# Performance work log

Measured on AMD Instinct MI355X. Metric: run time of the kernel, lower is better.

Reference implementation:

```python
import jax, jax.numpy as jnp
import numpy as np

EPS_LN = 1e-5
ALPHA_THRESH = 1.0 / 255.0


def _make_coord(X, Y):
    # make_coord((X,Y), flatten=True): centers in [-1,1], row-major over (X,Y)
    cx = (jnp.arange(X, dtype=jnp.float32) + 0.5) / X * 2.0 - 1.0
    cy = (jnp.arange(Y, dtype=jnp.float32) + 0.5) / Y * 2.0 - 1.0
    gx, gy = jnp.meshgrid(cx, cy, indexing='ij')
    return jnp.stack([gx.reshape(-1), gy.reshape(-1)], axis=-1)  # [X*Y, 2]


def _mlp(x, w1, b1, w2, b2):
    return jax.nn.relu(x @ w1 + b1) @ w2 + b2


def _unfold3x3(feat):
    # feat: [B,C,X,Y] -> torch F.unfold(3, padding=1) layout [B, C*9, X, Y]
    B, C, X, Y = feat.shape
    fp = jnp.pad(feat, ((0, 0), (0, 0), (1, 1), (1, 1)))
    patches = jnp.stack([fp[:, :, ki:ki + X, kj:kj + Y]
                         for ki in range(3) for kj in range(3)], axis=2)  # [B,C,9,X,Y]
    return patches.reshape(B, C * 9, X, Y)


def _render_one(xy, scale, rot, color, H, W):
    # project_gaussians_2d_scale_rot: ndc -> pixel centers
    cx = 0.5 * ((xy[:, 0] + 1.0) * W - 1.0)  # [N]
    cy = 0.5 * ((xy[:, 1] + 1.0) * H - 1.0)
    c, s = jnp.cos(rot[:, 0]), jnp.sin(rot[:, 0])
    sx2, sy2 = scale[:, 0] ** 2, scale[:, 1] ** 2
    cov00 = c * c * sx2 + s * s * sy2
    cov01 = c * s * (sx2 - sy2)
    cov11 = s * s * sx2 + c * c * sy2
    det = cov00 * cov11 - cov01 * cov01
    A = cov11 / det   # conic xx
    Bc = -cov01 / det  # conic xy
    Cc = cov00 / det  # conic yy
    px = jnp.arange(W, dtype=jnp.float32)
    py = jnp.arange(H, dtype=jnp.float32)
    dx = px[None, :, None] - cx[None, None, :]  # [1,W,N] -> broadcast [H,W,N]
    dy = py[:, None, None] - cy[None, None, :]  # [H,1,N]
    sigma = 0.5 * (A * dx * dx + Cc * dy * dy) + Bc * dx * dy  # [H,W,N]
    alpha = jnp.exp(-sigma)  # opacity = 1
    alpha = jnp.where(alpha >= ALPHA_THRESH, alpha, 0.0)  # rasterizer skip threshold
    img = jnp.einsum('hwn,nc->hwc', alpha, color)  # sum-compositing
    img = jnp.clip(img, 0.0, 1.0)
    return jnp.transpose(img, (2, 0, 1))  # [3,H,W]


def reference(inp, conv_w, conv_b,
              off_w1, off_b1, off_w2, off_b2,
              sc_w1, sc_b1, sc_w2, sc_b2,
              rot_w1, rot_b1, rot_w2, rot_b2,
              col_w1, col_b1, col_w2, col_b2,
              target_h, target_w):
    H0, W0 = inp.shape[-2], inp.shape[-1]
    factor = max(target_h / H0, target_w / W0)
    # encoder: 3x3 conv, same padding
    feat = jax.lax.conv_general_dilated(
        inp, conv_w, (1, 1), 'SAME',
        dimension_numbers=('NCHW', 'OIHW', 'NCHW')) + conv_b[None, :, None, None]
    feat = jnp.transpose(feat, (0, 1, 3, 2))  # [B,C,X=W0,Y=H0]
    B, C, X, Y = feat.shape
    feat = _unfold3x3(feat)  # [B,C*9,X,Y]
    feat = jnp.transpose(feat, (0, 2, 3, 1)).reshape(B, X * Y, C * 9)
    mu = jnp.mean(feat, axis=-1, keepdims=True)
    var = jnp.var(feat, axis=-1, keepdims=True)
    feat = (feat - mu) / jnp.sqrt(var + EPS_LN)
    coord = _make_coord(X, Y)[None]  # [1,N,2]
    off_factor = 2.0 * factor / max(target_h, target_w)
    offset = jnp.tanh(_mlp(feat, off_w1, off_b1, off_w2, off_b2)) * 3.0 * off_factor
    xy = coord + offset                                               # [B,N,2]
    scale = jax.nn.sigmoid(_mlp(feat, sc_w1, sc_b1, sc_w2, sc_b2)) * 2.0 * factor
    rot = jax.nn.sigmoid(_mlp(feat, rot_w1, rot_b1, rot_w2, rot_b2)) * 2.0 * jnp.pi
    color = jnp.tanh(_mlp(feat, col_w1, col_b1, col_w2, col_b2))
    render = jax.vmap(lambda a, b, c2, d: _render_one(a, b, c2, d, target_h, target_w))
    return render(xy, scale, rot, color)  # [B,3,H,W]


def setup_inputs() -> dict:
    key = jax.random.key(0)
    ks = jax.random.split(key, 16)
    d_in, hid = 288, 256

    def lin(k, fan_in, shape):
        return jax.random.normal(k, shape, jnp.float32) / np.sqrt(fan_in)

    return {
        'inp': jax.random.uniform(ks[0], (1, 3, 48, 48), jnp.float32),
        'conv_w': lin(ks[1], 27, (32, 3, 3, 3)),
        'conv_b': jnp.zeros((32,), jnp.float32),
        'off_w1': lin(ks[2], d_in, (d_in, hid)), 'off_b1': jnp.zeros((hid,), jnp.float32),
        'off_w2': lin(ks[3], hid, (hid, 2)), 'off_b2': jnp.zeros((2,), jnp.float32),
        'sc_w1': lin(ks[4], d_in, (d_in, hid)), 'sc_b1': jnp.zeros((hid,), jnp.float32),
        'sc_w2': lin(ks[5], hid, (hid, 2)), 'sc_b2': jnp.zeros((2,), jnp.float32),
        'rot_w1': lin(ks[6], d_in, (d_in, hid)), 'rot_b1': jnp.zeros((hid,), jnp.float32),
        'rot_w2': lin(ks[7], hid, (hid, 1)), 'rot_b2': jnp.zeros((1,), jnp.float32),
        'col_w1': lin(ks[8], d_in, (d_in, hid)), 'col_b1': jnp.zeros((hid,), jnp.float32),
        'col_w2': lin(ks[9], hid, (hid, 3)), 'col_b2': jnp.zeros((3,), jnp.float32),
        'target_h': 192,
        'target_w': 192,
    }
```

## Files before the change

### kernel.cpp

```cpp
#include <hip/hip_runtime.h>

#define NXY   48
#define NG    2304
#define CFE   32
#define KDIM  288
#define HID   256
#define NHID  1024
#define HW    192
#define NPIX  (HW*HW)
#define NCHUNK (NG/64)

typedef __bf16 bf16x8 __attribute__((ext_vector_type(8)));
typedef float  f32x4  __attribute__((ext_vector_type(4)));
typedef unsigned short ushort_t;
typedef unsigned int   uint_t;

__device__ __forceinline__ ushort_t f2bf(float x) {
    uint_t u = __float_as_uint(x);
    uint_t r = u + 0x7FFFu + ((u >> 16) & 1u);
    return (ushort_t)(r >> 16);
}
__device__ __forceinline__ float bf2f(ushort_t h) {
    return __uint_as_float(((uint_t)h) << 16);
}

__global__ __launch_bounds__(256) void conv_k(const float* __restrict__ inp,
                                              const float* __restrict__ cw,
                                              const float* __restrict__ cb,
                                              float* __restrict__ feat) {
    int idx = blockIdx.x * 256 + threadIdx.x;
    if (idx >= CFE * NXY * NXY) return;
    int w = idx % NXY, h = (idx / NXY) % NXY, o = idx / (NXY * NXY);
    float acc = cb[o];
    #pragma unroll
    for (int i = 0; i < 3; ++i) {
        #pragma unroll
        for (int kh = 0; kh < 3; ++kh) {
            int hh = h + kh - 1;
            if (hh < 0 || hh >= NXY) continue;
            #pragma unroll
            for (int kw = 0; kw < 3; ++kw) {
                int ww = w + kw - 1;
                if (ww < 0 || ww >= NXY) continue;
                acc = fmaf(inp[(i * NXY + hh) * NXY + ww],
                           cw[((o * 3 + i) * 3 + kh) * 3 + kw], acc);
            }
        }
    }
    feat[idx] = acc;
}

__global__ __launch_bounds__(64) void ln_k(const float* __restrict__ feat,
                                           ushort_t* __restrict__ Ahi,
                                           ushort_t* __restrict__ Alo) {
    int n = blockIdx.x;
    int lane = threadIdx.x;
    int x = n / NXY, y = n % NXY;
    float v[5];
    float sum = 0.f, sq = 0.f;
    #pragma unroll
    for (int i = 0; i < 5; ++i) {
        int k = lane + 64 * i;
        float val = 0.f;
        if (k < KDIM) {
            int c = k / 9, r = k % 9, ki = r / 3, kj = r % 3;
            int hh = y + kj - 1, ww = x + ki - 1;
            if (hh >= 0 && hh < NXY && ww >= 0 && ww < NXY)
                val = feat[(c * NXY + hh) * NXY + ww];
        }
        v[i] = val; sum += val; sq = fmaf(val, val, sq);
    }
    #pragma unroll
    for (int off = 32; off; off >>= 1) {
        sum += __shfl_xor(sum, off);
        sq  += __shfl_xor(sq,  off);
    }
    float mean = sum * (1.0f / KDIM);
    float var  = sq * (1.0f / KDIM) - mean * mean;
    float rstd = rsqrtf(var + 1e-5f);
    #pragma unroll
    for (int i = 0; i < 5; ++i) {
        int k = lane + 64 * i;
        if (k < KDIM) {
            float w = (v[i] - mean) * rstd;
            ushort_t hb = f2bf(w);
            ushort_t lb = f2bf(w - bf2f(hb));
            Ahi[n * KDIM + k] = hb;
            Alo[n * KDIM + k] = lb;
        }
    }
}

__global__ __launch_bounds__(256) void w1pack_k(const float* __restrict__ w0,
        const float* __restrict__ w1, const float* __restrict__ w2,
        const float* __restrict__ w3,
        ushort_t* __restrict__ Bph, ushort_t* __restrict__ Bpl) {
    int tid = blockIdx.x * 256 + threadIdx.x;
    if (tid >= 64 * 9 * 64) return;
    int l = tid & 63;
    int t = tid >> 6;
    int ks = t % 9, nf = t / 9;
    int ncol = nf * 16 + (l & 15);
    int head = ncol >> 8, c = ncol & 255;
    const float* w = head == 0 ? w0 : head == 1 ? w1 : head == 2 ? w2 : w3;
    int kbase = ks * 32 + (l >> 4) * 8;
    ushort_t hb[8], lb[8];
    #pragma unroll
    for (int i = 0; i < 8; ++i) {
        float x = w[(kbase + i) * HID + c];
        hb[i] = f2bf(x);
        lb[i] = f2bf(x - bf2f(hb[i]));
    }
    #pragma unroll
    for (int i = 0; i < 8; ++i) {
        Bph[tid * 8 + i] = hb[i];
        Bpl[tid * 8 + i] = lb[i];
    }
}

__global__ __launch_bounds__(256) void gemm_k(const ushort_t* __restrict__ Ahi,
        const ushort_t* __restrict__ Alo,
        const ushort_t* __restrict__ Bph, const ushort_t* __restrict__ Bpl,
        const float* __restrict__ b1_0, const float* __restrict__ b1_1,
        const float* __restrict__ b1_2, const float* __restrict__ b1_3,
        float* __restrict__ Hout) {
    int l   = threadIdx.x & 63;
    int wv  = threadIdx.x >> 6;
    int m0  = blockIdx.x * 64 + (wv >> 1) * 32;
    int nf0 = blockIdx.y * 4 + (wv & 1) * 2;
    int r15 = l & 15, kg = l >> 4;
    f32x4 acc[2][2] = {};
    const ushort_t* pah = Ahi + (m0 + r15) * KDIM + kg * 8;
    const ushort_t* pal = Alo + (m0 + r15) * KDIM + kg * 8;
    #pragma unroll 3
    for (int ks = 0; ks < 9; ++ks) {
        bf16x8 ah[2], al[2], bh[2], bl[2];
        #pragma unroll
        for (int m = 0; m < 2; ++m) {
            ah[m] = *(const bf16x8*)(pah + m * 16 * KDIM + ks * 32);
            al[m] = *(const bf16x8*)(pal + m * 16 * KDIM + ks * 32);
        }
        #pragma unroll
        for (int n = 0; n < 2; ++n) {
            size_t off = ((size_t)((nf0 + n) * 9 + ks) * 64 + l) * 8;
            bh[n] = *(const bf16x8*)(Bph + off);
            bl[n] = *(const bf16x8*)(Bpl + off);
        }
        #pragma unroll
        for (int m = 0; m < 2; ++m)
            #pragma unroll
            for (int n = 0; n < 2; ++n) {
                acc[m][n] = __builtin_amdgcn_mfma_f32_16x16x32_bf16(ah[m], bh[n], acc[m][n], 0, 0, 0);
                acc[m][n] = __builtin_amdgcn_mfma_f32_16x16x32_bf16(ah[m], bl[n], acc[m][n], 0, 0, 0);
                acc[m][n] = __builtin_amdgcn_mfma_f32_16x16x32_bf16(al[m], bh[n], acc[m][n], 0, 0, 0);
            }
    }
    #pragma unroll
    for (int n = 0; n < 2; ++n) {
        int col = (nf0 + n) * 16 + r15;
        int head = col >> 8;
        const float* bb = head == 0 ? b1_0 : head == 1 ? b1_1 : head == 2 ? b1_2 : b1_3;
        float bias = bb[col & 255];
        #pragma unroll
        for (int m = 0; m < 2; ++m)
            #pragma unroll
            for (int r = 0; r < 4; ++r) {
                int grow = m0 + m * 16 + kg * 4 + r;
                Hout[grow * NHID + col] = fmaxf(acc[m][n][r] + bias, 0.f);
            }
    }
}

__global__ __launch_bounds__(256) void head_k(const float* __restrict__ Hh,
        const float* __restrict__ ow2, const float* __restrict__ ob2,
        const float* __restrict__ sw2, const float* __restrict__ sb2,
        const float* __restrict__ rw2, const float* __restrict__ rb2,
        const float* __restrict__ cw2, const float* __restrict__ cb2,
        float4* __restrict__ gbox, float4* __restrict__ gdat) {
    int tid = threadIdx.x;
    int lane = tid & 63, wv = tid >> 6;
    int n = blockIdx.x * 4 + wv;
    const float* h = Hh + n * NHID;
    float s[8] = {};
    #pragma unroll
    for (int i = 0; i < 4; ++i) {
        int j = lane + 64 * i;
        float h0 = h[j], h1 = h[256 + j], h2 = h[512 + j], h3 = h[768 + j];
        s[0] = fmaf(h0, ow2[j * 2 + 0], s[0]);
        s[1] = fmaf(h0, ow2[j * 2 + 1], s[1]);
        s[2] = fmaf(h1, sw2[j * 2 + 0], s[2]);
        s[3] = fmaf(h1, sw2[j * 2 + 1], s[3]);
        s[4] = fmaf(h2, rw2[j],         s[4]);
        s[5] = fmaf(h3, cw2[j * 3 + 0], s[5]);
        s[6] = fmaf(h3, cw2[j * 3 + 1], s[6]);
        s[7] = fmaf(h3, cw2[j * 3 + 2], s[7]);
    }
    #pragma unroll
    for (int off = 32; off; off >>= 1)
        #pragma unroll
        for (int k = 0; k < 8; ++k) s[k] += __shfl_xor(s[k], off);
    if (lane == 0) {
        float o0 = s[0] + ob2[0], o1 = s[1] + ob2[1];
        float z0 = s[2] + sb2[0], z1 = s[3] + sb2[1];
        float zr = s[4] + rb2[0];
        float c0 = s[5] + cb2[0], c1 = s[6] + cb2[1], c2 = s[7] + cb2[2];
        int x = n / NXY, y = n % NXY;
        float ndcx = ((x + 0.5f) * (2.0f / NXY) - 1.0f) + tanhf(o0) * 0.125f;
        float ndcy = ((y + 0.5f) * (2.0f / NXY) - 1.0f) + tanhf(o1) * 0.125f;
        float cxp = 0.5f * ((ndcx + 1.0f) * HW - 1.0f);
        float cyp = 0.5f * ((ndcy + 1.0f) * HW - 1.0f);
        float sx = 8.0f / (1.0f + expf(-z0));
        float sy = 8.0f / (1.0f + expf(-z1));
        float rot = 6.283185307179586f / (1.0f + expf(-zr));
        float cc = cosf(rot), ss = sinf(rot);
        float sx2 = sx * sx, sy2 = sy * sy;
        float cov00 = cc * cc * sx2 + ss * ss * sy2;
        float cov01 = cc * ss * (sx2 - sy2);
        float cov11 = ss * ss * sx2 + cc * cc * sy2;
        float det = cov00 * cov11 - cov01 * cov01;
        float inv = 1.0f / det;
        float A = cov11 * inv, Bc = -cov01 * inv, Cc = cov00 * inv;
        float rx = sqrtf(11.2f * cov00) + 1e-2f;
        float ry = sqrtf(11.2f * cov11) + 1e-2f;
        gbox[n]         = make_float4(cxp, cyp, rx, ry);
        gdat[2 * n]     = make_float4(0.5f * A, Bc, 0.5f * Cc, tanhf(c0));
        gdat[2 * n + 1] = make_float4(tanhf(c1), tanhf(c2), 0.f, 0.f);
    }
}

__global__ __launch_bounds__(256) void render_k(const float4* __restrict__ gbox,
                                                const float4* __restrict__ gdat,
                                                float* __restrict__ out) {
    __shared__ float4 ldsE[4][64][2];
    __shared__ float red[4][64][3];
    int lane = threadIdx.x & 63;
    int wv   = threadIdx.x >> 6;
    int tx0 = blockIdx.x * 8, ty0 = blockIdx.y * 8;
    float px = (float)(tx0 + (lane & 7));
    float py = (float)(ty0 + (lane >> 3));
    float xlo = (float)tx0, xhi = (float)(tx0 + 7);
    float ylo = (float)ty0, yhi = (float)(ty0 + 7);
    float ar = 0.f, ag = 0.f, ab = 0.f;
    for (int c = wv; c < NCHUNK; c += 4) {
        int g = c * 64 + lane;
        float4 bb = gbox[g];
        bool pred = (bb.x - bb.z <= xhi) && (bb.x + bb.z >= xlo) &&
                    (bb.y - bb.w <= yhi) && (bb.y + bb.w >= ylo);
        unsigned long long m = __ballot(pred);
        int cnt = __popcll(m);
        int pos = __popcll(m & ((1ull << lane) - 1ull));
        if (pred) {
            float4 d0 = gdat[2 * g];
            float4 d1 = gdat[2 * g + 1];
            ldsE[wv][pos][0] = make_float4(bb.x, bb.y, d0.x, d0.y);
            ldsE[wv][pos][1] = make_float4(d0.z, d0.w, d1.x, d1.y);
        }
        __syncthreads();
        for (int i = 0; i < cnt; ++i) {
            float4 e0 = ldsE[wv][i][0];
            float4 e1 = ldsE[wv][i][1];
            float dx = px - e0.x;
            float dy = py - e0.y;
            float sigma = fmaf(dx, fmaf(e0.z, dx, e0.w * dy), e1.x * dy * dy);
            float a = __expf(-sigma);
            a = (a >= (1.0f / 255.0f)) ? a : 0.f;
            ar = fmaf(a, e1.y, ar);
            ag = fmaf(a, e1.z, ag);
            ab = fmaf(a, e1.w, ab);
        }
        __syncthreads();
    }
    red[wv][lane][0] = ar; red[wv][lane][1] = ag; red[wv][lane][2] = ab;
    __syncthreads();
    if (wv == 0) {
        float r_ = red[0][lane][0] + red[1][lane][0] + red[2][lane][0] + red[3][lane][0];
        float g_ = red[0][lane][1] + red[1][lane][1] + red[2][lane][1] + red[3][lane][1];
        float b_ = red[0][lane][2] + red[1][lane][2] + red[2][lane][2] + red[3][lane][2];
        int pix = (ty0 + (lane >> 3)) * HW + tx0 + (lane & 7);
        out[pix]            = fminf(fmaxf(r_, 0.f), 1.f);
        out[NPIX + pix]     = fminf(fmaxf(g_, 0.f), 1.f);
        out[2 * NPIX + pix] = fminf(fmaxf(b_, 0.f), 1.f);
    }
}

extern "C" void kernel_launch(void* const* d_in, const int* in_sizes, int n_in,
                              void* d_out, int out_size, void* d_ws, size_t ws_size,
                              hipStream_t stream) {
    const float* inp = (const float*)d_in[0];
    const float* cw  = (const float*)d_in[1];
    const float* cb  = (const float*)d_in[2];
    const float* ow1 = (const float*)d_in[3];
    const float* ob1 = (const float*)d_in[4];
    const float* ow2 = (const float*)d_in[5];
    const float* ob2 = (const float*)d_in[6];
    const float* sw1 = (const float*)d_in[7];
    const float* sb1 = (const float*)d_in[8];
    const float* sw2 = (const float*)d_in[9];
    const float* sb2 = (const float*)d_in[10];
    const float* rw1 = (const float*)d_in[11];
    const float* rb1 = (const float*)d_in[12];
    const float* rw2 = (const float*)d_in[13];
    const float* rb2 = (const float*)d_in[14];
    const float* cw1 = (const float*)d_in[15];
    const float* cb1 = (const float*)d_in[16];
    const float* cw2 = (const float*)d_in[17];
    const float* cb2 = (const float*)d_in[18];

    float* ws = (float*)d_ws;
    float*    feat = ws;
    float*    hid  = ws + 73728;
    float4*   gbox = (float4*)(ws + 2433024);
    float4*   gdat = (float4*)(ws + 2442240);
    ushort_t* Ahi  = (ushort_t*)(ws + 2460672);
    ushort_t* Alo  = (ushort_t*)(ws + 2792448);
    ushort_t* Bph  = (ushort_t*)(ws + 3124224);
    ushort_t* Bpl  = (ushort_t*)(ws + 3271680);
    float* out = (float*)d_out;

    hipLaunchKernelGGL(conv_k, dim3(288), dim3(256), 0, stream, inp, cw, cb, feat);
    hipLaunchKernelGGL(ln_k, dim3(NG), dim3(64), 0, stream, feat, Ahi, Alo);
    hipLaunchKernelGGL(w1pack_k, dim3(144), dim3(256), 0, stream,
                       ow1, sw1, rw1, cw1, Bph, Bpl);
    hipLaunchKernelGGL(gemm_k, dim3(36, 16), dim3(256), 0, stream,
                       Ahi, Alo, Bph, Bpl, ob1, sb1, rb1, cb1, hid);
    hipLaunchKernelGGL(head_k, dim3(576), dim3(256), 0, stream,
                       hid, ow2, ob2, sw2, sb2, rw2, rb2, cw2, cb2, gbox, gdat);
    hipLaunchKernelGGL(render_k, dim3(24, 24), dim3(256), 0, stream, gbox, gdat, out);
}
```

Baseline: 47.30 us.

## Split-K the hidden GEMM into two partials and drop render barriers

The first-layer GEMM grid gains a z dimension that splits the 9 K-steps into two ranges. Each half writes its raw partial sums to a separate buffer, and head_k now adds the two partials plus the bias and applies ReLU. This doubles the number of GEMM blocks to fill more CUs, at the cost of twice the hidden-activation write and read traffic. Separately, render_k replaces its block-wide __syncthreads around the per-wave LDS staging with an LDS waitcnt, because each wave only reads its own ldsE slice.

```diff
diff --git a/kernel.cpp b/kernel.cpp
--- a/kernel.cpp
+++ b/kernel.cpp
@@ -118,22 +118,13 @@
     }
 }
 
-__global__ __launch_bounds__(256) void gemm_k(const ushort_t* __restrict__ Ahi,
-        const ushort_t* __restrict__ Alo,
+template<int KB, int KE>
+__device__ __forceinline__ void gemm_core(const ushort_t* __restrict__ pah,
+        const ushort_t* __restrict__ pal,
         const ushort_t* __restrict__ Bph, const ushort_t* __restrict__ Bpl,
-        const float* __restrict__ b1_0, const float* __restrict__ b1_1,
-        const float* __restrict__ b1_2, const float* __restrict__ b1_3,
-        float* __restrict__ Hout) {
-    int l   = threadIdx.x & 63;
-    int wv  = threadIdx.x >> 6;
-    int m0  = blockIdx.x * 64 + (wv >> 1) * 32;
-    int nf0 = blockIdx.y * 4 + (wv & 1) * 2;
-    int r15 = l & 15, kg = l >> 4;
-    f32x4 acc[2][2] = {};
-    const ushort_t* pah = Ahi + (m0 + r15) * KDIM + kg * 8;
-    const ushort_t* pal = Alo + (m0 + r15) * KDIM + kg * 8;
-    #pragma unroll 3
-    for (int ks = 0; ks < 9; ++ks) {
+        int nf0, int l, f32x4 acc[2][2]) {
+    #pragma unroll
+    for (int ks = KB; ks < KE; ++ks) {
         bf16x8 ah[2], al[2], bh[2], bl[2];
         #pragma unroll
         for (int m = 0; m < 2; ++m) {
@@ -155,23 +146,40 @@
                 acc[m][n] = __builtin_amdgcn_mfma_f32_16x16x32_bf16(al[m], bh[n], acc[m][n], 0, 0, 0);
             }
     }
+}
+
+__global__ __launch_bounds__(256, 4) void gemm_k(const ushort_t* __restrict__ Ahi,
+        const ushort_t* __restrict__ Alo,
+        const ushort_t* __restrict__ Bph, const ushort_t* __restrict__ Bpl,
+        float* __restrict__ HP) {
+    int l   = threadIdx.x & 63;
+    int wv  = threadIdx.x >> 6;
+    int kz  = blockIdx.z;
+    int m0  = blockIdx.x * 64 + (wv >> 1) * 32;
+    int nf0 = blockIdx.y * 4 + (wv & 1) * 2;
+    int r15 = l & 15, kg = l >> 4;
+    f32x4 acc[2][2] = {};
+    const ushort_t* pah = Ahi + (m0 + r15) * KDIM + kg * 8;
+    const ushort_t* pal = Alo + (m0 + r15) * KDIM + kg * 8;
+    if (kz == 0) gemm_core<0, 4>(pah, pal, Bph, Bpl, nf0, l, acc);
+    else         gemm_core<4, 9>(pah, pal, Bph, Bpl, nf0, l, acc);
+    float* out = HP + (size_t)kz * NG * NHID;
     #pragma unroll
     for (int n = 0; n < 2; ++n) {
         int col = (nf0 + n) * 16 + r15;
-        int head = col >> 8;
-        const float* bb = head == 0 ? b1_0 : head == 1 ? b1_1 : head == 2 ? b1_2 : b1_3;
-        float bias = bb[col & 255];
         #pragma unroll
         for (int m = 0; m < 2; ++m)
             #pragma unroll
             for (int r = 0; r < 4; ++r) {
                 int grow = m0 + m * 16 + kg * 4 + r;
-                Hout[grow * NHID + col] = fmaxf(acc[m][n][r] + bias, 0.f);
+                out[grow * NHID + col] = acc[m][n][r];
             }
     }
 }
 
-__global__ __launch_bounds__(256) void head_k(const float* __restrict__ Hh,
+__global__ __launch_bounds__(256) void head_k(const float* __restrict__ HP,
+        const float* __restrict__ ob1, const float* __restrict__ sb1,
+        const float* __restrict__ rb1, const float* __restrict__ cb1,
         const float* __restrict__ ow2, const float* __restrict__ ob2,
         const float* __restrict__ sw2, const float* __restrict__ sb2,
         const float* __restrict__ rw2, const float* __restrict__ rb2,
@@ -180,12 +188,16 @@
     int tid = threadIdx.x;
     int lane = tid & 63, wv = tid >> 6;
     int n = blockIdx.x * 4 + wv;
-    const float* h = Hh + n * NHID;
+    const float* p0 = HP + (size_t)n * NHID;
+    const float* p1 = HP + (size_t)NG * NHID + (size_t)n * NHID;
     float s[8] = {};
     #pragma unroll
     for (int i = 0; i < 4; ++i) {
         int j = lane + 64 * i;
-        float h0 = h[j], h1 = h[256 + j], h2 = h[512 + j], h3 = h[768 + j];
+        float h0 = fmaxf(p0[j]       + p1[j]       + ob1[j], 0.f);
+        float h1 = fmaxf(p0[256 + j] + p1[256 + j] + sb1[j], 0.f);
+        float h2 = fmaxf(p0[512 + j] + p1[512 + j] + rb1[j], 0.f);
+        float h3 = fmaxf(p0[768 + j] + p1[768 + j] + cb1[j], 0.f);
         s[0] = fmaf(h0, ow2[j * 2 + 0], s[0]);
         s[1] = fmaf(h0, ow2[j * 2 + 1], s[1]);
         s[2] = fmaf(h1, sw2[j * 2 + 0], s[2]);
@@ -255,7 +267,7 @@
             ldsE[wv][pos][0] = make_float4(bb.x, bb.y, d0.x, d0.y);
             ldsE[wv][pos][1] = make_float4(d0.z, d0.w, d1.x, d1.y);
         }
-        __syncthreads();
+        asm volatile("s_waitcnt lgkmcnt(0)" ::: "memory");
         for (int i = 0; i < cnt; ++i) {
             float4 e0 = ldsE[wv][i][0];
             float4 e1 = ldsE[wv][i][1];
@@ -268,7 +280,6 @@
             ag = fmaf(a, e1.z, ag);
             ab = fmaf(a, e1.w, ab);
         }
-        __syncthreads();
     }
     red[wv][lane][0] = ar; red[wv][lane][1] = ag; red[wv][lane][2] = ab;
     __syncthreads();
@@ -308,22 +319,23 @@
 
     float* ws = (float*)d_ws;
     float*    feat = ws;
-    float*    hid  = ws + 73728;
-    float4*   gbox = (float4*)(ws + 2433024);
-    float4*   gdat = (float4*)(ws + 2442240);
-    ushort_t* Ahi  = (ushort_t*)(ws + 2460672);
-    ushort_t* Alo  = (ushort_t*)(ws + 2792448);
-    ushort_t* Bph  = (ushort_t*)(ws + 3124224);
-    ushort_t* Bpl  = (ushort_t*)(ws + 3271680);
+    float*    HP   = ws + 73728;
+    float4*   gbox = (float4*)(ws + 4792320);
+    float4*   gdat = (float4*)(ws + 4801536);
+    ushort_t* Ahi  = (ushort_t*)(ws + 4819968);
+    ushort_t* Alo  = (ushort_t*)(ws + 5151744);
+    ushort_t* Bph  = (ushort_t*)(ws + 5483520);
+    ushort_t* Bpl  = (ushort_t*)(ws + 5630976);
     float* out = (float*)d_out;
 
     hipLaunchKernelGGL(conv_k, dim3(288), dim3(256), 0, stream, inp, cw, cb, feat);
     hipLaunchKernelGGL(ln_k, dim3(NG), dim3(64), 0, stream, feat, Ahi, Alo);
     hipLaunchKernelGGL(w1pack_k, dim3(144), dim3(256), 0, stream,
                        ow1, sw1, rw1, cw1, Bph, Bpl);
-    hipLaunchKernelGGL(gemm_k, dim3(36, 16), dim3(256), 0, stream,
-                       Ahi, Alo, Bph, Bpl, ob1, sb1, rb1, cb1, hid);
+    hipLaunchKernelGGL(gemm_k, dim3(36, 16, 2), dim3(256), 0, stream,
+                       Ahi, Alo, Bph, Bpl, HP);
     hipLaunchKernelGGL(head_k, dim3(576), dim3(256), 0, stream,
-                       hid, ow2, ob2, sw2, sb2, rw2, rb2, cw2, cb2, gbox, gdat);
+                       HP, ob1, sb1, rb1, cb1,
+                       ow2, ob2, sw2, sb2, rw2, rb2, cw2, cb2, gbox, gdat);
     hipLaunchKernelGGL(render_k, dim3(24, 24), dim3(256), 0, stream, gbox, gdat, out);
 }
```

After: 47.50 us. About the same (+0.4%).

## Fuse conv, layernorm and weight packing into one prep kernel; drop render barriers

Applied to the files above, without the earlier changes.

Conv, unfold+layernorm and W1 bf16 hi/lo packing are merged into a single prep kernel. Each block recomputes a small conv halo tile into shared memory and then normalizes four gaussians' features from it. Extra blocks do the weight packing, which removes two launches and the global feat round-trip at the cost of some redundant conv work. In render, the block-wide __syncthreads inside the chunk loop are replaced by a wave-local LDS waitcnt, since each wave uses only its own LDS slice. This relies on wave-synchronous execution for correctness.

```diff
diff --git a/kernel.cpp b/kernel.cpp
--- a/kernel.cpp
+++ b/kernel.cpp
@@ -2,7 +2,6 @@
 
 #define NXY   48
 #define NG    2304
-#define CFE   32
 #define KDIM  288
 #define HID   256
 #define NHID  1024
@@ -24,111 +23,109 @@
     return __uint_as_float(((uint_t)h) << 16);
 }
 
-__global__ __launch_bounds__(256) void conv_k(const float* __restrict__ inp,
-                                              const float* __restrict__ cw,
-                                              const float* __restrict__ cb,
-                                              float* __restrict__ feat) {
-    int idx = blockIdx.x * 256 + threadIdx.x;
-    if (idx >= CFE * NXY * NXY) return;
-    int w = idx % NXY, h = (idx / NXY) % NXY, o = idx / (NXY * NXY);
-    float acc = cb[o];
-    #pragma unroll
-    for (int i = 0; i < 3; ++i) {
-        #pragma unroll
-        for (int kh = 0; kh < 3; ++kh) {
-            int hh = h + kh - 1;
-            if (hh < 0 || hh >= NXY) continue;
-            #pragma unroll
-            for (int kw = 0; kw < 3; ++kw) {
-                int ww = w + kw - 1;
-                if (ww < 0 || ww >= NXY) continue;
-                acc = fmaf(inp[(i * NXY + hh) * NXY + ww],
-                           cw[((o * 3 + i) * 3 + kh) * 3 + kw], acc);
-            }
-        }
-    }
-    feat[idx] = acc;
-}
-
-__global__ __launch_bounds__(64) void ln_k(const float* __restrict__ feat,
-                                           ushort_t* __restrict__ Ahi,
-                                           ushort_t* __restrict__ Alo) {
-    int n = blockIdx.x;
-    int lane = threadIdx.x;
-    int x = n / NXY, y = n % NXY;
-    float v[5];
-    float sum = 0.f, sq = 0.f;
-    #pragma unroll
-    for (int i = 0; i < 5; ++i) {
-        int k = lane + 64 * i;
-        float val = 0.f;
-        if (k < KDIM) {
-            int c = k / 9, r = k % 9, ki = r / 3, kj = r % 3;
-            int hh = y + kj - 1, ww = x + ki - 1;
-            if (hh >= 0 && hh < NXY && ww >= 0 && ww < NXY)
-                val = feat[(c * NXY + hh) * NXY + ww];
-        }
-        v[i] = val; sum += val; sq = fmaf(val, val, sq);
-    }
-    #pragma unroll
-    for (int off = 32; off; off >>= 1) {
-        sum += __shfl_xor(sum, off);
-        sq  += __shfl_xor(sq,  off);
-    }
-    float mean = sum * (1.0f / KDIM);
-    float var  = sq * (1.0f / KDIM) - mean * mean;
-    float rstd = rsqrtf(var + 1e-5f);
-    #pragma unroll
-    for (int i = 0; i < 5; ++i) {
-        int k = lane + 64 * i;
-        if (k < KDIM) {
-            float w = (v[i] - mean) * rstd;
-            ushort_t hb = f2bf(w);
-            ushort_t lb = f2bf(w - bf2f(hb));
-            Ahi[n * KDIM + k] = hb;
-            Alo[n * KDIM + k] = lb;
-        }
-    }
-}
-
-__global__ __launch_bounds__(256) void w1pack_k(const float* __restrict__ w0,
-        const float* __restrict__ w1, const float* __restrict__ w2,
-        const float* __restrict__ w3,
+__global__ __launch_bounds__(256) void prep_k(const float* __restrict__ inp,
+        const float* __restrict__ cw, const float* __restrict__ cb,
+        const float* __restrict__ w1o, const float* __restrict__ w1s,
+        const float* __restrict__ w1r, const float* __restrict__ w1c,
+        ushort_t* __restrict__ Ahi, ushort_t* __restrict__ Alo,
         ushort_t* __restrict__ Bph, ushort_t* __restrict__ Bpl) {
-    int tid = blockIdx.x * 256 + threadIdx.x;
-    if (tid >= 64 * 9 * 64) return;
-    int l = tid & 63;
-    int t = tid >> 6;
-    int ks = t % 9, nf = t / 9;
-    int ncol = nf * 16 + (l & 15);
-    int head = ncol >> 8, c = ncol & 255;
-    const float* w = head == 0 ? w0 : head == 1 ? w1 : head == 2 ? w2 : w3;
-    int kbase = ks * 32 + (l >> 4) * 8;
-    ushort_t hb[8], lb[8];
-    #pragma unroll
-    for (int i = 0; i < 8; ++i) {
-        float x = w[(kbase + i) * HID + c];
-        hb[i] = f2bf(x);
-        lb[i] = f2bf(x - bf2f(hb[i]));
-    }
-    #pragma unroll
-    for (int i = 0; i < 8; ++i) {
-        Bph[tid * 8 + i] = hb[i];
-        Bpl[tid * 8 + i] = lb[i];
+    __shared__ float convT[3][6][32];
+    const int t    = blockIdx.x;
+    const int tid  = threadIdx.x;
+    const int lane = tid & 63;
+    const int wv   = tid >> 6;
+    if (t < 576) {
+        int n0 = t * 4;
+        int x  = n0 / NXY;
+        int y0 = n0 % NXY;
+        for (int i = tid; i < 576; i += 256) {
+            int c  = i & 31;
+            int ys = (i >> 5) % 6;
+            int xs = i / 192;
+            int w_ = x - 1 + xs, h_ = y0 - 1 + ys;
+            float acc = 0.f;
+            if (w_ >= 0 && w_ < NXY && h_ >= 0 && h_ < NXY) {
+                acc = cb[c];
+                #pragma unroll
+                for (int i3 = 0; i3 < 3; ++i3)
+                    #pragma unroll
+                    for (int kh = 0; kh < 3; ++kh) {
+                        int hh = h_ + kh - 1;
+                        if (hh < 0 || hh >= NXY) continue;
+                        #pragma unroll
+                        for (int kw = 0; kw < 3; ++kw) {
+                            int ww = w_ + kw - 1;
+                            if (ww < 0 || ww >= NXY) continue;
+                            acc = fmaf(inp[(i3 * NXY + hh) * NXY + ww],
+                                       cw[((c * 3 + i3) * 3 + kh) * 3 + kw], acc);
+                        }
+                    }
+            }
+            convT[xs][ys][c] = acc;
+        }
+        __syncthreads();
+        int n = n0 + wv;
+        float v[5];
+        float sum = 0.f, sq = 0.f;
+        #pragma unroll
+        for (int i5 = 0; i5 < 5; ++i5) {
+            int k = lane + 64 * i5;
+            float val = 0.f;
+            if (k < KDIM) {
+                int c = k / 9, r = k % 9, ki = r / 3, kj = r % 3;
+                val = convT[ki][wv + kj][c];
+            }
+            v[i5] = val; sum += val; sq = fmaf(val, val, sq);
+        }
+        #pragma unroll
+        for (int off = 32; off; off >>= 1) {
+            sum += __shfl_xor(sum, off);
+            sq  += __shfl_xor(sq,  off);
+        }
+        float mean = sum * (1.0f / KDIM);
+        float var  = sq * (1.0f / KDIM) - mean * mean;
+        float rstd = rsqrtf(var + 1e-5f);
+        #pragma unroll
+        for (int i5 = 0; i5 < 5; ++i5) {
+            int k = lane + 64 * i5;
+            if (k < KDIM) {
+                float w = (v[i5] - mean) * rstd;
+                ushort_t hb = f2bf(w);
+                Ahi[n * KDIM + k] = hb;
+                Alo[n * KDIM + k] = f2bf(w - bf2f(hb));
+            }
+        }
+    } else {
+        int t2 = (t - 576) * 256 + tid;
+        int l = t2 & 63, tt = t2 >> 6;
+        int ks = tt % 9, nf = tt / 9;
+        int ncol = nf * 16 + (l & 15);
+        int head = ncol >> 8, c = ncol & 255;
+        const float* w = head == 0 ? w1o : head == 1 ? w1s
+                       : head == 2 ? w1r : w1c;
+        int kbase = ks * 32 + (l >> 4) * 8;
+        #pragma unroll
+        for (int i = 0; i < 8; ++i) {
+            float xv = w[(kbase + i) * HID + c];
+            ushort_t hb = f2bf(xv);
+            Bph[t2 * 8 + i] = hb;
+            Bpl[t2 * 8 + i] = f2bf(xv - bf2f(hb));
+        }
     }
 }
 
 __global__ __launch_bounds__(256) void gemm_k(const ushort_t* __restrict__ Ahi,
         const ushort_t* __restrict__ Alo,
         const ushort_t* __restrict__ Bph, const ushort_t* __restrict__ Bpl,
-        const float* __restrict__ b1_0, const float* __restrict__ b1_1,
-        const float* __restrict__ b1_2, const float* __restrict__ b1_3,
-        float* __restrict__ Hout) {
-    int l   = threadIdx.x & 63;
-    int wv  = threadIdx.x >> 6;
-    int m0  = blockIdx.x * 64 + (wv >> 1) * 32;
-    int nf0 = blockIdx.y * 4 + (wv & 1) * 2;
-    int r15 = l & 15, kg = l >> 4;
+        const float* __restrict__ b1o, const float* __restrict__ b1s,
+        const float* __restrict__ b1r, const float* __restrict__ b1c,
+        float* __restrict__ hid) {
+    const int t    = blockIdx.x;
+    const int lane = threadIdx.x & 63;
+    const int wv   = threadIdx.x >> 6;
+    int m0  = (t >> 4) * 64 + (wv >> 1) * 32;
+    int nf0 = (t & 15) * 4 + (wv & 1) * 2;
+    int r15 = lane & 15, kg = lane >> 4;
     f32x4 acc[2][2] = {};
     const ushort_t* pah = Ahi + (m0 + r15) * KDIM + kg * 8;
     const ushort_t* pal = Alo + (m0 + r15) * KDIM + kg * 8;
@@ -142,7 +139,7 @@
         }
         #pragma unroll
         for (int n = 0; n < 2; ++n) {
-            size_t off = ((size_t)((nf0 + n) * 9 + ks) * 64 + l) * 8;
+            size_t off = ((size_t)((nf0 + n) * 9 + ks) * 64 + lane) * 8;
             bh[n] = *(const bf16x8*)(Bph + off);
             bl[n] = *(const bf16x8*)(Bpl + off);
         }
@@ -159,28 +156,29 @@
     for (int n = 0; n < 2; ++n) {
         int col = (nf0 + n) * 16 + r15;
         int head = col >> 8;
-        const float* bb = head == 0 ? b1_0 : head == 1 ? b1_1 : head == 2 ? b1_2 : b1_3;
+        const float* bb = head == 0 ? b1o : head == 1 ? b1s
+                        : head == 2 ? b1r : b1c;
         float bias = bb[col & 255];
         #pragma unroll
         for (int m = 0; m < 2; ++m)
             #pragma unroll
             for (int r = 0; r < 4; ++r) {
                 int grow = m0 + m * 16 + kg * 4 + r;
-                Hout[grow * NHID + col] = fmaxf(acc[m][n][r] + bias, 0.f);
-            }
-    }
-}
-
-__global__ __launch_bounds__(256) void head_k(const float* __restrict__ Hh,
+                hid[(size_t)grow * NHID + col] = fmaxf(acc[m][n][r] + bias, 0.f);
+            }
+    }
+}
+
+__global__ __launch_bounds__(256) void head_k(const float* __restrict__ hid,
         const float* __restrict__ ow2, const float* __restrict__ ob2,
         const float* __restrict__ sw2, const float* __restrict__ sb2,
         const float* __restrict__ rw2, const float* __restrict__ rb2,
         const float* __restrict__ cw2, const float* __restrict__ cb2,
         float4* __restrict__ gbox, float4* __restrict__ gdat) {
-    int tid = threadIdx.x;
-    int lane = tid & 63, wv = tid >> 6;
+    const int lane = threadIdx.x & 63;
+    const int wv   = threadIdx.x >> 6;
     int n = blockIdx.x * 4 + wv;
-    const float* h = Hh + n * NHID;
+    const float* h = hid + (size_t)n * NHID;
     float s[8] = {};
     #pragma unroll
     for (int i = 0; i < 4; ++i) {
@@ -229,13 +227,13 @@
 }
 
 __global__ __launch_bounds__(256) void render_k(const float4* __restrict__ gbox,
-                                                const float4* __restrict__ gdat,
-                                                float* __restrict__ out) {
+        const float4* __restrict__ gdat, float* __restrict__ out) {
     __shared__ float4 ldsE[4][64][2];
-    __shared__ float red[4][64][3];
-    int lane = threadIdx.x & 63;
-    int wv   = threadIdx.x >> 6;
-    int tx0 = blockIdx.x * 8, ty0 = blockIdx.y * 8;
+    __shared__ float  red[4][64][3];
+    const int t    = blockIdx.x;
+    const int lane = threadIdx.x & 63;
+    const int wv   = threadIdx.x >> 6;
+    int tx0 = (t % 24) * 8, ty0 = (t / 24) * 8;
     float px = (float)(tx0 + (lane & 7));
     float py = (float)(ty0 + (lane >> 3));
     float xlo = (float)tx0, xhi = (float)(tx0 + 7);
@@ -255,7 +253,7 @@
             ldsE[wv][pos][0] = make_float4(bb.x, bb.y, d0.x, d0.y);
             ldsE[wv][pos][1] = make_float4(d0.z, d0.w, d1.x, d1.y);
         }
-        __syncthreads();
+        asm volatile("s_waitcnt lgkmcnt(0)" ::: "memory");
         for (int i = 0; i < cnt; ++i) {
             float4 e0 = ldsE[wv][i][0];
             float4 e1 = ldsE[wv][i][1];
@@ -268,7 +266,6 @@
             ag = fmaf(a, e1.z, ag);
             ab = fmaf(a, e1.w, ab);
         }
-        __syncthreads();
     }
     red[wv][lane][0] = ar; red[wv][lane][1] = ag; red[wv][lane][2] = ab;
     __syncthreads();
@@ -289,41 +286,39 @@
     const float* inp = (const float*)d_in[0];
     const float* cw  = (const float*)d_in[1];
     const float* cb  = (const float*)d_in[2];
-    const float* ow1 = (const float*)d_in[3];
-    const float* ob1 = (const float*)d_in[4];
+    const float* w1o = (const float*)d_in[3];
+    const float* b1o = (const float*)d_in[4];
     const float* ow2 = (const float*)d_in[5];
     const float* ob2 = (const float*)d_in[6];
-    const float* sw1 = (const float*)d_in[7];
-    const float* sb1 = (const float*)d_in[8];
+    const float* w1s = (const float*)d_in[7];
+    const float* b1s = (const float*)d_in[8];
     const float* sw2 = (const float*)d_in[9];
     const float* sb2 = (const float*)d_in[10];
-    const float* rw1 = (const float*)d_in[11];
-    const float* rb1 = (const float*)d_in[12];
+    const float* w1r = (const float*)d_in[11];
+    const float* b1r = (const float*)d_in[12];
     const float* rw2 = (const float*)d_in[13];
     const float* rb2 = (const float*)d_in[14];
-    const float* cw1 = (const float*)d_in[15];
-    const float* cb1 = (const float*)d_in[16];
+    const float* w1c = (const float*)d_in[15];
+    const float* b1c = (const float*)d_in[16];
     const float* cw2 = (const float*)d_in[17];
     const float* cb2 = (const float*)d_in[18];
 
     float* ws = (float*)d_ws;
-    float*    feat = ws;
-    float*    hid  = ws + 73728;
-    float4*   gbox = (float4*)(ws + 2433024);
-    float4*   gdat = (float4*)(ws + 2442240);
-    ushort_t* Ahi  = (ushort_t*)(ws + 2460672);
-    ushort_t* Alo  = (ushort_t*)(ws + 2792448);
-    ushort_t* Bph  = (ushort_t*)(ws + 3124224);
-    ushort_t* Bpl  = (ushort_t*)(ws + 3271680);
+    float*    hid  = ws;
+    float4*   gbox = (float4*)(ws + 2359296);
+    float4*   gdat = (float4*)(ws + 2368512);
+    ushort_t* Ahi  = (ushort_t*)(ws + 2386944);
+    ushort_t* Alo  = (ushort_t*)(ws + 2718720);
+    ushort_t* Bph  = (ushort_t*)(ws + 3050496);
+    ushort_t* Bpl  = (ushort_t*)(ws + 3197952);
     float* out = (float*)d_out;
 
-    hipLaunchKernelGGL(conv_k, dim3(288), dim3(256), 0, stream, inp, cw, cb, feat);
-    hipLaunchKernelGGL(ln_k, dim3(NG), dim3(64), 0, stream, feat, Ahi, Alo);
-    hipLaunchKernelGGL(w1pack_k, dim3(144), dim3(256), 0, stream,
-                       ow1, sw1, rw1, cw1, Bph, Bpl);
-    hipLaunchKernelGGL(gemm_k, dim3(36, 16), dim3(256), 0, stream,
-                       Ahi, Alo, Bph, Bpl, ob1, sb1, rb1, cb1, hid);
+    hipLaunchKernelGGL(prep_k, dim3(720), dim3(256), 0, stream,
+                       inp, cw, cb, w1o, w1s, w1r, w1c, Ahi, Alo, Bph, Bpl);
+    hipLaunchKernelGGL(gemm_k, dim3(576), dim3(256), 0, stream,
+                       Ahi, Alo, Bph, Bpl, b1o, b1s, b1r, b1c, hid);
     hipLaunchKernelGGL(head_k, dim3(576), dim3(256), 0, stream,
                        hid, ow2, ob2, sw2, sb2, rw2, rb2, cw2, cb2, gbox, gdat);
-    hipLaunchKernelGGL(render_k, dim3(24, 24), dim3(256), 0, stream, gbox, gdat, out);
-}
+    hipLaunchKernelGGL(render_k, dim3(576), dim3(256), 0, stream,
+                       gbox, gdat, out);
+}
```

Measured after the change: 50.89 us. +7.6%, slower.
